# Optimization experiments

Measured on AMD Instinct MI355X. Metric: run time of the kernel, lower is better.

Reference implementation:

```python
import jax, jax.numpy as jnp
import numpy as np

B, C, D, H, W = 2, 128, 16, 96, 96


def setup_inputs() -> dict:
    key = jax.random.key(0)
    k1, k2 = jax.random.split(key)
    x = jax.random.normal(k1, (B, C, D, H, W), dtype=jnp.float32)
    gamma = jax.random.uniform(k2, (1,), dtype=jnp.float32)
    return {"x": x, "gamma": gamma}


def reference(x, gamma):
    b, c, d, h, w = x.shape
    n = d * h * w
    q = x.reshape(b, c, n)                      # [B,C,N] query==key==value
    # energy: [B,C,C] = q @ q^T
    energy = jnp.einsum('bcn,bdn->bcd', q, q)
    # EnergyMaxNorm: rowwise max (AdaptiveMaxPool1d(1) over last dim) minus energy
    e_max = jnp.max(energy, axis=-1, keepdims=True)
    energy = e_max - energy
    attn = jax.nn.softmax(energy, axis=-1)      # [B,C,C]
    out = jnp.einsum('bcd,bdn->bcn', attn, q)   # [B,C,N]
    out = out.reshape(b, c, d, h, w)
    # gamma-scaled residual fusion (modulation_type 'addition')
    return x + gamma[0] * out
```

## Files before the change

### kernel.cpp

```cpp
#include <hip/hip_runtime.h>

typedef unsigned short u16;
typedef unsigned int u32;
typedef __attribute__((ext_vector_type(8))) short short8;
typedef __attribute__((ext_vector_type(4))) float f32x4;
typedef __attribute__((ext_vector_type(4))) u16 u16x4;

#define NBATCH 2
#define NC 128
#define NN 147456
#define CH 64
#define NCH (NN / CH)
#define G1_PARTS 256
#define N3_PER_B 1152

__device__ __forceinline__ u16 bf16rne(float f) {
  u32 u = __builtin_bit_cast(u32, f);
  return (u16)((u + 0x7FFFu + ((u >> 16) & 1u)) >> 16);
}
__device__ __forceinline__ float bf2f(u16 h) {
  u32 u = ((u32)h) << 16;
  return __builtin_bit_cast(float, u);
}
__device__ __forceinline__ void split2(float f, u16& h, u16& g) {
  u32 u = __builtin_bit_cast(u32, f);
  h = (u16)(u >> 16);
  float hf = __builtin_bit_cast(float, u & 0xFFFF0000u);
  g = bf16rne(f - hf);
}

__global__ __launch_bounds__(256, 2)
void gram_k(const float* __restrict__ x, float* __restrict__ part) {
  __shared__ u16 hi[2][128 * CH];
  __shared__ u16 lo[2][128 * CH];
  const int tid = threadIdx.x;
  const int bid = blockIdx.x;
  const int b   = bid >> 8;
  const int pi  = bid & 255;
  const int w   = tid >> 6;
  const int l   = tid & 63;
  const int grp = l >> 4;
  const int lr  = l & 15;
  const int swz = (lr & 7) << 3;
  const float* xb = x + (size_t)b * NC * NN;

  const int col4 = tid & 15;
  const int r0   = tid >> 4;

  f32x4 acc[2][8];
#pragma unroll
  for (int i = 0; i < 2; ++i)
#pragma unroll
    for (int j = 0; j < 8; ++j) acc[i][j] = (f32x4){0.f, 0.f, 0.f, 0.f};

  float4 v[8];

  auto issue = [&](int ch) {
    const int k0 = ch * CH + (col4 << 2);
#pragma unroll
    for (int j = 0; j < 8; ++j)
      v[j] = *(const float4*)(xb + (size_t)(r0 + (j << 4)) * NN + k0);
  };
  auto stage = [&](int bb) {
    u16* H = &hi[bb][0];
    u16* L = &lo[bb][0];
#pragma unroll
    for (int j = 0; j < 8; ++j) {
      const int row = r0 + (j << 4);
      const int idx = (row << 6) + ((col4 << 2) ^ ((row & 7) << 3));
      u16 h0, h1, h2, h3, g0, g1, g2, g3;
      split2(v[j].x, h0, g0); split2(v[j].y, h1, g1);
      split2(v[j].z, h2, g2); split2(v[j].w, h3, g3);
      *(u16x4*)(H + idx) = (u16x4){h0, h1, h2, h3};
      *(u16x4*)(L + idx) = (u16x4){g0, g1, g2, g3};
    }
  };
  const int m0 = (w << 5) + lr;
  const int m1 = m0 + 16;
  auto mma = [&](int bb) {
    const u16* H = &hi[bb][0];
    const u16* L = &lo[bb][0];
#pragma unroll
    for (int kk = 0; kk < CH; kk += 32) {
      const int kv = (kk + (grp << 3)) ^ swz;
      const short8 Ah0 = *(const short8*)(H + (m0 << 6) + kv);
      const short8 Al0 = *(const short8*)(L + (m0 << 6) + kv);
      const short8 Ah1 = *(const short8*)(H + (m1 << 6) + kv);
      const short8 Al1 = *(const short8*)(L + (m1 << 6) + kv);
#pragma unroll
      for (int nt = 0; nt < 8; ++nt) {
        const int nr  = (nt << 4) + lr;
        const int bix = (nr << 6) + kv;
        const short8 Bh = *(const short8*)(H + bix);
        const short8 Bl = *(const short8*)(L + bix);
        acc[0][nt] = __builtin_amdgcn_mfma_f32_16x16x32_bf16(Ah0, Bh, acc[0][nt], 0, 0, 0);
        acc[0][nt] = __builtin_amdgcn_mfma_f32_16x16x32_bf16(Ah0, Bl, acc[0][nt], 0, 0, 0);
        acc[0][nt] = __builtin_amdgcn_mfma_f32_16x16x32_bf16(Al0, Bh, acc[0][nt], 0, 0, 0);
        acc[1][nt] = __builtin_amdgcn_mfma_f32_16x16x32_bf16(Ah1, Bh, acc[1][nt], 0, 0, 0);
        acc[1][nt] = __builtin_amdgcn_mfma_f32_16x16x32_bf16(Ah1, Bl, acc[1][nt], 0, 0, 0);
        acc[1][nt] = __builtin_amdgcn_mfma_f32_16x16x32_bf16(Al1, Bh, acc[1][nt], 0, 0, 0);
      }
    }
  };

  issue(pi);
  stage(0);
  __syncthreads();

  const int NITER = NCH / G1_PARTS;
  for (int i = 0; i < NITER; ++i) {
    if (i + 1 < NITER) issue(pi + (i + 1) * G1_PARTS);
    mma(i & 1);
    if (i + 1 < NITER) stage((i + 1) & 1);
    __syncthreads();
  }

  float* pb = part + (size_t)bid * 16384;
#pragma unroll
  for (int mt = 0; mt < 2; ++mt)
#pragma unroll
    for (int nt = 0; nt < 8; ++nt)
#pragma unroll
      for (int r = 0; r < 4; ++r) {
        const int row = (w << 5) + (mt << 4) + (grp << 2) + r;
        const int col = (nt << 4) + lr;
        pb[(row << 7) + col] = acc[mt][nt][r];
      }
}

__global__ __launch_bounds__(128)
void soft_k(const float* __restrict__ part, u16* __restrict__ attn) {
  const int b = blockIdx.x >> 7;
  const int c = blockIdx.x & 127;
  const int d = threadIdx.x;
  __shared__ float red[128];
  float e = 0.f;
  const float* p0 = part + ((size_t)(b * G1_PARTS) << 14) + (c << 7) + d;
  for (int p = 0; p < G1_PARTS; ++p) e += p0[(size_t)p << 14];
  red[d] = e;
  __syncthreads();
#pragma unroll
  for (int s = 64; s > 0; s >>= 1) {
    if (d < s) red[d] = fminf(red[d], red[d + s]);
    __syncthreads();
  }
  const float emin = red[0];
  __syncthreads();
  const float pr = __expf(emin - e);
  red[d] = pr;
  __syncthreads();
#pragma unroll
  for (int s = 64; s > 0; s >>= 1) {
    if (d < s) red[d] += red[d + s];
    __syncthreads();
  }
  const float inv = 1.f / red[0];
  attn[(((size_t)b) << 14) + (c << 7) + d] = bf16rne(pr * inv);
}

__global__ __launch_bounds__(256, 4)
void pv_k(const float* __restrict__ x, const u16* __restrict__ attn,
          const float* __restrict__ gamma, float* __restrict__ out) {
  __shared__ u16 at[128 * 128];
  const int tid = threadIdx.x;
  const int bid = blockIdx.x;
  const int b   = bid / N3_PER_B;
  const int nb  = (bid % N3_PER_B) << 7;
  const int w = tid >> 6, l = tid & 63, grp = l >> 4, lr = l & 15;
  const int swz = lr << 3;
  const size_t bbase = (size_t)b * NC * NN;
  const u16* ab = attn + ((size_t)b << 14);

#pragma unroll
  for (int j = 0; j < 8; ++j) {
    const int idx = (j << 8) + tid;
    const int c  = idx >> 4;
    const int d0 = (idx & 15) << 3;
    const int dst = (c << 7) + (d0 ^ ((c & 15) << 3));
    *(short8*)(at + dst) = *(const short8*)(ab + (c << 7) + d0);
  }
  __syncthreads();

  f32x4 acc[8][2];
#pragma unroll
  for (int i = 0; i < 8; ++i) {
    acc[i][0] = (f32x4){0.f, 0.f, 0.f, 0.f};
    acc[i][1] = (f32x4){0.f, 0.f, 0.f, 0.f};
  }

  const int n0 = nb + (w << 5) + lr;
#pragma unroll
  for (int kk = 0; kk < 128; kk += 32) {
    const int d0 = kk + (grp << 3);
    short8 Bh[2];
#pragma unroll
    for (int t = 0; t < 2; ++t) {
      const int n = n0 + (t << 4);
      const float* src = x + bbase + (size_t)d0 * NN + n;
      float f[8];
#pragma unroll
      for (int i = 0; i < 8; ++i) f[i] = src[(size_t)i * NN];
      u16 h[8];
#pragma unroll
      for (int i = 0; i < 8; ++i) h[i] = bf16rne(f[i]);
      Bh[t] = (short8){(short)h[0], (short)h[1], (short)h[2], (short)h[3],
                       (short)h[4], (short)h[5], (short)h[6], (short)h[7]};
    }
#pragma unroll
    for (int mt = 0; mt < 8; ++mt) {
      const int mrow = (mt << 4) + lr;
      const short8 Ah = *(const short8*)(at + (mrow << 7) + ((kk + (grp << 3)) ^ swz));
#pragma unroll
      for (int t = 0; t < 2; ++t)
        acc[mt][t] = __builtin_amdgcn_mfma_f32_16x16x32_bf16(Ah, Bh[t], acc[mt][t], 0, 0, 0);
    }
  }

  const float gm = gamma[0];
#pragma unroll
  for (int mt = 0; mt < 8; ++mt)
#pragma unroll
    for (int t = 0; t < 2; ++t)
#pragma unroll
      for (int r = 0; r < 4; ++r) {
        const int c = (mt << 4) + (grp << 2) + r;
        const int n = n0 + (t << 4);
        const size_t off = bbase + (size_t)c * NN + n;
        out[off] = x[off] + gm * acc[mt][t][r];
      }
}

extern "C" void kernel_launch(void* const* d_in, const int* in_sizes, int n_in,
                              void* d_out, int out_size, void* d_ws, size_t ws_size,
                              hipStream_t stream) {
  (void)in_sizes; (void)n_in; (void)out_size; (void)ws_size;
  const float* x     = (const float*)d_in[0];
  const float* gamma = (const float*)d_in[1];
  float* out  = (float*)d_out;
  u16*   attn = (u16*)d_ws;
  float* part = out;

  gram_k<<<dim3(2 * G1_PARTS), dim3(256), 0, stream>>>(x, part);
  soft_k<<<dim3(2 * 128),      dim3(128), 0, stream>>>(part, attn);
  pv_k  <<<dim3(2 * N3_PER_B), dim3(256), 0, stream>>>(x, attn, gamma, out);
}
```

Measured before the change: 115.7 us.

## Split PV kernel into 32-column tiles with eight waves over channel rows

The PV kernel now processes 32 spatial columns per block using 512 threads. Each wave computes a 16-row channel slice instead of all 128 rows over 32 columns, so each wave holds 2 accumulators instead of 16. The aim is more parallelism and lower register pressure. In exchange, all eight waves in a block read and convert the same x columns. With four times as many blocks, the 32 KB attention matrix is also loaded into LDS four times as often, adding redundant memory traffic.

```diff
diff --git a/kernel.cpp b/kernel.cpp
--- a/kernel.cpp
+++ b/kernel.cpp
@@ -12,7 +12,8 @@
 #define CH 64
 #define NCH (NN / CH)
 #define G1_PARTS 256
-#define N3_PER_B 1152
+#define PVN 32
+#define PV_PER_B (NN / PVN)
 
 __device__ __forceinline__ u16 bf16rne(float f) {
   u32 u = __builtin_bit_cast(u32, f);
@@ -158,22 +159,22 @@
   attn[(((size_t)b) << 14) + (c << 7) + d] = bf16rne(pr * inv);
 }
 
-__global__ __launch_bounds__(256, 4)
+__global__ __launch_bounds__(512, 8)
 void pv_k(const float* __restrict__ x, const u16* __restrict__ attn,
           const float* __restrict__ gamma, float* __restrict__ out) {
   __shared__ u16 at[128 * 128];
   const int tid = threadIdx.x;
   const int bid = blockIdx.x;
-  const int b   = bid / N3_PER_B;
-  const int nb  = (bid % N3_PER_B) << 7;
+  const int b   = bid / PV_PER_B;
+  const int nb  = (bid % PV_PER_B) << 5;
   const int w = tid >> 6, l = tid & 63, grp = l >> 4, lr = l & 15;
   const int swz = lr << 3;
   const size_t bbase = (size_t)b * NC * NN;
   const u16* ab = attn + ((size_t)b << 14);
 
 #pragma unroll
-  for (int j = 0; j < 8; ++j) {
-    const int idx = (j << 8) + tid;
+  for (int j = 0; j < 4; ++j) {
+    const int idx = (j << 9) + tid;
     const int c  = idx >> 4;
     const int d0 = (idx & 15) << 3;
     const int dst = (c << 7) + (d0 ^ ((c & 15) << 3));
@@ -181,21 +182,18 @@
   }
   __syncthreads();
 
-  f32x4 acc[8][2];
-#pragma unroll
-  for (int i = 0; i < 8; ++i) {
-    acc[i][0] = (f32x4){0.f, 0.f, 0.f, 0.f};
-    acc[i][1] = (f32x4){0.f, 0.f, 0.f, 0.f};
-  }
-
-  const int n0 = nb + (w << 5) + lr;
+  f32x4 acc[2];
+  acc[0] = (f32x4){0.f, 0.f, 0.f, 0.f};
+  acc[1] = (f32x4){0.f, 0.f, 0.f, 0.f};
+
+  const int mrow = (w << 4) + lr;
 #pragma unroll
   for (int kk = 0; kk < 128; kk += 32) {
     const int d0 = kk + (grp << 3);
-    short8 Bh[2];
+    const short8 Ah = *(const short8*)(at + (mrow << 7) + ((kk + (grp << 3)) ^ swz));
 #pragma unroll
     for (int t = 0; t < 2; ++t) {
-      const int n = n0 + (t << 4);
+      const int n = nb + (t << 4) + lr;
       const float* src = x + bbase + (size_t)d0 * NN + n;
       float f[8];
 #pragma unroll
@@ -203,31 +201,22 @@
       u16 h[8];
 #pragma unroll
       for (int i = 0; i < 8; ++i) h[i] = bf16rne(f[i]);
-      Bh[t] = (short8){(short)h[0], (short)h[1], (short)h[2], (short)h[3],
-                       (short)h[4], (short)h[5], (short)h[6], (short)h[7]};
-    }
-#pragma unroll
-    for (int mt = 0; mt < 8; ++mt) {
-      const int mrow = (mt << 4) + lr;
-      const short8 Ah = *(const short8*)(at + (mrow << 7) + ((kk + (grp << 3)) ^ swz));
-#pragma unroll
-      for (int t = 0; t < 2; ++t)
-        acc[mt][t] = __builtin_amdgcn_mfma_f32_16x16x32_bf16(Ah, Bh[t], acc[mt][t], 0, 0, 0);
+      const short8 Bh = (short8){(short)h[0], (short)h[1], (short)h[2], (short)h[3],
+                                 (short)h[4], (short)h[5], (short)h[6], (short)h[7]};
+      acc[t] = __builtin_amdgcn_mfma_f32_16x16x32_bf16(Ah, Bh, acc[t], 0, 0, 0);
     }
   }
 
   const float gm = gamma[0];
 #pragma unroll
-  for (int mt = 0; mt < 8; ++mt)
-#pragma unroll
-    for (int t = 0; t < 2; ++t)
-#pragma unroll
-      for (int r = 0; r < 4; ++r) {
-        const int c = (mt << 4) + (grp << 2) + r;
-        const int n = n0 + (t << 4);
-        const size_t off = bbase + (size_t)c * NN + n;
-        out[off] = x[off] + gm * acc[mt][t][r];
-      }
+  for (int t = 0; t < 2; ++t)
+#pragma unroll
+    for (int r = 0; r < 4; ++r) {
+      const int c = (w << 4) + (grp << 2) + r;
+      const int n = nb + (t << 4) + lr;
+      const size_t off = bbase + (size_t)c * NN + n;
+      out[off] = x[off] + gm * acc[t][r];
+    }
 }
 
 extern "C" void kernel_launch(void* const* d_in, const int* in_sizes, int n_in,
@@ -242,5 +231,5 @@
 
   gram_k<<<dim3(2 * G1_PARTS), dim3(256), 0, stream>>>(x, part);
   soft_k<<<dim3(2 * 128),      dim3(128), 0, stream>>>(part, attn);
-  pv_k  <<<dim3(2 * N3_PER_B), dim3(256), 0, stream>>>(x, attn, gamma, out);
-}
+  pv_k  <<<dim3(NBATCH * PV_PER_B), dim3(512), 0, stream>>>(x, attn, gamma, out);
+}
```

After: 133.6 us. +15.4%, slower.
